# Kernel tuning notes

Measured on AMD Instinct MI355X. Metric: run time of the kernel, lower is better.

The kernel has to match this reference:

```python
import jax, jax.numpy as jnp
import numpy as np

N = 20000      # nodes
E = 320000     # edges (before self-loops)
IN = 128       # input_dim
HID = 64       # hidden_dim
HEADS = 4      # num_heads
SLOPE = 0.2    # PyG GATConv leaky_relu negative_slope


def setup_inputs() -> dict:
    key = jax.random.key(0)
    ks = jax.random.split(key, 20)
    g = lambda k, shape: jax.random.normal(k, shape, dtype=jnp.float32) * 0.1
    return {
        "x": jax.random.normal(ks[0], (N, IN), dtype=jnp.float32),
        "edge_index": jax.random.randint(ks[1], (2, E), 0, N),
        # layer 0: IN -> HID x HEADS, concat
        "lin0": g(ks[2], (IN, HEADS * HID)),
        "att_src0": g(ks[3], (HEADS, HID)),
        "att_dst0": g(ks[4], (HEADS, HID)),
        "bias0": g(ks[5], (HEADS * HID,)),
        # layer 1: HID*HEADS -> HID x HEADS, concat
        "lin1": g(ks[6], (HEADS * HID, HEADS * HID)),
        "att_src1": g(ks[7], (HEADS, HID)),
        "att_dst1": g(ks[8], (HEADS, HID)),
        "bias1": g(ks[9], (HEADS * HID,)),
        # layer 2: HID*HEADS -> HID, 1 head, mean (concat=False)
        "lin2": g(ks[10], (HEADS * HID, HID)),
        "att_src2": g(ks[11], (1, HID)),
        "att_dst2": g(ks[12], (1, HID)),
        "bias2": g(ks[13], (HID,)),
        # output MLP: HID -> HID//2 -> 1
        "w1": g(ks[14], (HID, HID // 2)),
        "b1": g(ks[15], (HID // 2,)),
        "w2": g(ks[16], (HID // 2, 1)),
        "b2": g(ks[17], (1,)),
    }


def _gat(x, src, dst, lin, att_src, att_dst, bias, heads, concat):
    n = x.shape[0]
    ch = att_src.shape[1]
    h = (x @ lin).reshape(n, heads, ch)                       # [N,H,C]
    a_s = jnp.sum(h * att_src, axis=-1)                       # [N,H]
    a_d = jnp.sum(h * att_dst, axis=-1)                       # [N,H]
    e = jax.nn.leaky_relu(a_s[src] + a_d[dst], negative_slope=SLOPE)  # [E,H]
    emax = jax.ops.segment_max(e, dst, num_segments=n)        # segment softmax over dst
    ee = jnp.exp(e - emax[dst])
    denom = jax.ops.segment_sum(ee, dst, num_segments=n)
    alpha = ee / denom[dst]                                   # [E,H]
    out = jax.ops.segment_sum(h[src] * alpha[:, :, None], dst, num_segments=n)  # [N,H,C]
    out = out.reshape(n, heads * ch) if concat else jnp.mean(out, axis=1)
    return out + bias


def reference(x, edge_index, lin0, att_src0, att_dst0, bias0,
              lin1, att_src1, att_dst1, bias1,
              lin2, att_src2, att_dst2, bias2,
              w1, b1, w2, b2):
    n = x.shape[0]
    loops = jnp.arange(n, dtype=edge_index.dtype)
    edge = jnp.concatenate([edge_index, jnp.stack([loops, loops])], axis=1)  # add self loops
    src, dst = edge[0], edge[1]
    h = jax.nn.elu(_gat(x, src, dst, lin0, att_src0, att_dst0, bias0, HEADS, True))
    h = jax.nn.elu(_gat(h, src, dst, lin1, att_src1, att_dst1, bias1, HEADS, True))
    h = jax.nn.elu(_gat(h, src, dst, lin2, att_src2, att_dst2, bias2, 1, False))
    h = jax.nn.relu(h @ w1 + b1)
    return h @ w2 + b2
```

## Files before the change

### kernel.cpp

```cpp
#include <hip/hip_runtime.h>

#define NNODES 20000
#define NEDGES 320000
#define SCAN_NB ((NNODES + 255) / 256)
#define DCAP 120

typedef __attribute__((ext_vector_type(8))) short bf16x8;
typedef __attribute__((ext_vector_type(4))) float f32x4;
typedef _Float16 f16x4 __attribute__((ext_vector_type(4)));
typedef _Float16 f16x8 __attribute__((ext_vector_type(8)));

__device__ __forceinline__ float leaky(float x) { return x > 0.f ? x : 0.2f * x; }
__device__ __forceinline__ float elu(float x) { return x > 0.f ? x : expm1f(x); }

__device__ __forceinline__ ushort f2bf(float f) {
  uint u = __float_as_uint(f);
  uint r = (u + 0x7fffu + ((u >> 16) & 1u)) >> 16;
  return (ushort)r;
}
__device__ __forceinline__ float bf2f(ushort h) {
  return __uint_as_float(((uint)h) << 16);
}

__device__ __forceinline__ void gll16(const ushort* g, ushort* l) {
  __builtin_amdgcn_global_load_lds((const __attribute__((address_space(1))) void*)g,
                                   (__attribute__((address_space(3))) void*)l, 16, 0, 0);
}

__global__ void k_hist(const int* __restrict__ dst, int* __restrict__ cnt, int e) {
  int i = blockIdx.x * blockDim.x + threadIdx.x;
  if (i < e) atomicAdd(&cnt[dst[i]], 1);
}

__global__ __launch_bounds__(256) void k_scan1(const int* __restrict__ cnt, int* __restrict__ row_start,
                                               int* __restrict__ blocksum, int n) {
  __shared__ int s[256];
  int t = threadIdx.x;
  int i = blockIdx.x * 256 + t;
  int v = (i < n) ? cnt[i] : 0;
  s[t] = v;
  __syncthreads();
  for (int off = 1; off < 256; off <<= 1) {
    int x = (t >= off) ? s[t - off] : 0;
    __syncthreads();
    s[t] += x;
    __syncthreads();
  }
  if (i < n) row_start[i] = s[t] - v;
  if (t == 255) blocksum[blockIdx.x] = s[255];
}

__global__ __launch_bounds__(128) void k_scan2(int* __restrict__ blocksum, int* __restrict__ blockoff,
                                               int* __restrict__ row_start, int nb, int n) {
  __shared__ int s[128];
  int t = threadIdx.x;
  int v = (t < nb) ? blocksum[t] : 0;
  s[t] = v;
  __syncthreads();
  for (int off = 1; off < 128; off <<= 1) {
    int x = (t >= off) ? s[t - off] : 0;
    __syncthreads();
    s[t] += x;
    __syncthreads();
  }
  if (t < nb) blockoff[t] = s[t] - v;
  if (t == nb - 1) row_start[n] = s[t];
}

__global__ __launch_bounds__(256) void k_scan3(int* __restrict__ row_start, const int* __restrict__ blockoff,
                                               int* __restrict__ fill, int n) {
  int i = blockIdx.x * 256 + threadIdx.x;
  if (i < n) {
    row_start[i] += blockoff[blockIdx.x];
    fill[i] = 0;
  }
}

__global__ void k_scatter(const int* __restrict__ src, const int* __restrict__ dst,
                          const int* __restrict__ row_start, int* __restrict__ fill,
                          int* __restrict__ csr, int e) {
  int i = blockIdx.x * blockDim.x + threadIdx.x;
  if (i < e) {
    int d = dst[i];
    int p = row_start[d] + atomicAdd(&fill[d], 1);
    csr[p] = src[i];
  }
}

__global__ void k_cvt_pack(const float* __restrict__ a, ushort* __restrict__ hi,
                           ushort* __restrict__ lo, int total, int* __restrict__ fill) {
  int i = blockIdx.x * blockDim.x + threadIdx.x;
  if (i < NNODES) fill[i] = 0;
  if (i >= total) return;
  const float* src = a + (size_t)i * 32;
  ushort h[32], lw[32];
#pragma unroll
  for (int r = 0; r < 32; r++) {
    int p = (r < 16) ? ((r >> 2) * 8 + (r & 3)) : (((r - 16) >> 2) * 8 + 4 + (r & 3));
    float v = src[r];
    ushort hh = f2bf(v);
    h[p] = hh;
    lw[p] = f2bf(v - bf2f(hh));
  }
  ushort* ho = hi + (size_t)i * 32;
  ushort* llo = lo + (size_t)i * 32;
#pragma unroll
  for (int q = 0; q < 4; q++) {
    *(bf16x8*)&ho[q * 8] = *(bf16x8*)&h[q * 8];
    *(bf16x8*)&llo[q * 8] = *(bf16x8*)&lw[q * 8];
  }
}

__device__ __forceinline__ void prep_w_one(const float* __restrict__ w, ushort* __restrict__ th,
                                           ushort* __restrict__ tl, int K, int OC, int idx) {
  int KC = K / 32;
  int oc = idx / KC, c = idx % KC;
  ushort h[32], lw[32];
#pragma unroll
  for (int r = 0; r < 32; r++) {
    int p = (r < 16) ? ((r >> 2) * 8 + (r & 3)) : (((r - 16) >> 2) * 8 + 4 + (r & 3));
    float v = w[(size_t)(c * 32 + r) * OC + oc];
    ushort hh = f2bf(v);
    h[p] = hh;
    lw[p] = f2bf(v - bf2f(hh));
  }
  ushort* ho = th + (size_t)oc * K + c * 32;
  ushort* llo = tl + (size_t)oc * K + c * 32;
#pragma unroll
  for (int q = 0; q < 4; q++) {
    *(bf16x8*)&ho[q * 8] = *(bf16x8*)&h[q * 8];
    *(bf16x8*)&llo[q * 8] = *(bf16x8*)&lw[q * 8];
  }
}

__global__ void k_prep_w3(const float* __restrict__ w0, const float* __restrict__ w1,
                          const float* __restrict__ w2,
                          ushort* __restrict__ th0, ushort* __restrict__ tl0,
                          ushort* __restrict__ th1, ushort* __restrict__ tl1,
                          ushort* __restrict__ th2, ushort* __restrict__ tl2) {
  int i = blockIdx.x * blockDim.x + threadIdx.x;
  if (i < 1024) prep_w_one(w0, th0, tl0, 128, 256, i);
  else if (i < 3072) prep_w_one(w1, th1, tl1, 256, 256, i - 1024);
  else if (i < 3584) prep_w_one(w2, th2, tl2, 256, 64, i - 3072);
}

template <int K, int NCT, int HEADS>
__global__ __launch_bounds__(256) void k_gemm_mfma(const ushort* __restrict__ Ah, const ushort* __restrict__ Al,
                                                   const ushort* __restrict__ Bh, const ushort* __restrict__ Bl,
                                                   const float* __restrict__ asrc, const float* __restrict__ adst,
                                                   _Float16* __restrict__ H, float* __restrict__ a_s,
                                                   float* __restrict__ a_d, int M, int OC) {
  constexpr int BM = 64, BN = NCT * 64, NC = K / 32;
  constexpr int ALO = 2048;
  constexpr int BOFF = 4096;
  constexpr int BLO = BOFF + BN * 32;
  constexpr int BUFE = BOFF + BN * 64;
  __shared__ ushort sb0[BUFE], sb1[BUFE];
  __shared__ float sh_s[4][64], sh_d[4][64];
  int w = threadIdx.x >> 6, l = threadIdx.x & 63;
  int n0 = blockIdx.x * BM;
  int cw = blockIdx.y * BN + w * (NCT * 16);
  int lr = l & 15;

  int q = l & 3;
  int srow = 16 * w + (l >> 2);
  int sgrow = min(n0 + srow, M - 1);
  int gA = q ^ ((srow >> 1) & 3);
  const ushort* aH = Ah + (size_t)sgrow * K + gA * 8;
  const ushort* aL = Al + (size_t)sgrow * K + gA * 8;
  const ushort* bH[NCT];
  const ushort* bL[NCT];
  int colb[NCT];
#pragma unroll
  for (int i = 0; i < NCT; i++) {
    colb[i] = 16 * NCT * w + 16 * i;
    int sc = colb[i] + (l >> 2);
    int gB = q ^ ((sc >> 1) & 3);
    bH[i] = Bh + (size_t)(blockIdx.y * BN + sc) * K + gB * 8;
    bL[i] = Bl + (size_t)(blockIdx.y * BN + sc) * K + gB * 8;
  }

#define STAGE(buf, c)                                              \
  {                                                                \
    gll16(aH + (c) * 32, &buf[0 + w * 512]);                       \
    gll16(aL + (c) * 32, &buf[ALO + w * 512]);                     \
    _Pragma("unroll") for (int i = 0; i < NCT; i++) {              \
      gll16(bH[i] + (c) * 32, &buf[BOFF + colb[i] * 32]);          \
      gll16(bL[i] + (c) * 32, &buf[BLO + colb[i] * 32]);           \
    }                                                              \
  }

  f32x4 acc[4][NCT];
#pragma unroll
  for (int r = 0; r < 4; r++)
#pragma unroll
    for (int t = 0; t < NCT; t++) acc[r][t] = (f32x4){0.f, 0.f, 0.f, 0.f};

#define COMP(buf)                                                                   \
  {                                                                                 \
    bf16x8 bhf[NCT], blf[NCT];                                                      \
    _Pragma("unroll") for (int t = 0; t < NCT; t++) {                               \
      int bcol = 16 * NCT * w + 16 * t + lr;                                        \
      int gb = (l >> 4) ^ ((bcol >> 1) & 3);                                        \
      bhf[t] = *(const bf16x8*)&buf[BOFF + bcol * 32 + gb * 8];                     \
      blf[t] = *(const bf16x8*)&buf[BLO + bcol * 32 + gb * 8];                      \
    }                                                                               \
    _Pragma("unroll") for (int r = 0; r < 4; r++) {                                 \
      int arow = 16 * r + lr;                                                       \
      int ga = (l >> 4) ^ ((arow >> 1) & 3);                                        \
      bf16x8 ahf = *(const bf16x8*)&buf[arow * 32 + ga * 8];                        \
      bf16x8 alf = *(const bf16x8*)&buf[ALO + arow * 32 + ga * 8];                  \
      _Pragma("unroll") for (int t = 0; t < NCT; t++) {                             \
        acc[r][t] = __builtin_amdgcn_mfma_f32_16x16x32_bf16(ahf, bhf[t], acc[r][t], 0, 0, 0); \
        acc[r][t] = __builtin_amdgcn_mfma_f32_16x16x32_bf16(alf, bhf[t], acc[r][t], 0, 0, 0); \
        acc[r][t] = __builtin_amdgcn_mfma_f32_16x16x32_bf16(ahf, blf[t], acc[r][t], 0, 0, 0); \
      }                                                                             \
    }                                                                               \
  }

  ushort* cur = sb0;
  ushort* nxt = sb1;
  STAGE(cur, 0);
  __syncthreads();
  for (int c = 0; c < NC; ++c) {
    if (c + 1 < NC) STAGE(nxt, c + 1);
    COMP(cur);
    __syncthreads();
    ushort* tmp = cur; cur = nxt; nxt = tmp;
  }
#undef STAGE
#undef COMP

#pragma unroll
  for (int r = 0; r < 4; r++)
#pragma unroll
    for (int t = 0; t < NCT; t++)
#pragma unroll
      for (int reg = 0; reg < 4; reg++) {
        int row = n0 + 16 * r + (l >> 4) * 4 + reg;
        if (row < M) H[(size_t)row * OC + cw + 16 * t + lr] = (_Float16)acc[r][t][reg];
      }

  float asv[NCT], adv[NCT];
#pragma unroll
  for (int t = 0; t < NCT; t++) {
    asv[t] = asrc[cw + 16 * t + lr];
    adv[t] = adst[cw + 16 * t + lr];
  }
#pragma unroll
  for (int r = 0; r < 4; r++) {
#pragma unroll
    for (int reg = 0; reg < 4; reg++) {
      float ps = 0.f, pd = 0.f;
#pragma unroll
      for (int t = 0; t < NCT; t++) {
        ps += acc[r][t][reg] * asv[t];
        pd += acc[r][t][reg] * adv[t];
      }
#pragma unroll
      for (int mask = 1; mask < 16; mask <<= 1) {
        ps += __shfl_xor(ps, mask, 64);
        pd += __shfl_xor(pd, mask, 64);
      }
      int rl = 16 * r + (l >> 4) * 4 + reg;
      if (lr == 0) { sh_s[w][rl] = ps; sh_d[w][rl] = pd; }
    }
  }
  __syncthreads();
  int tid = threadIdx.x;
  if (HEADS == 4) {
    if (tid < 128) {
      int rr = tid & 63, hl = tid >> 6;
      int row = n0 + rr;
      if (row < M) {
        int hidx = row * 4 + blockIdx.y * 2 + hl;
        a_s[hidx] = sh_s[2 * hl][rr] + sh_s[2 * hl + 1][rr];
        a_d[hidx] = sh_d[2 * hl][rr] + sh_d[2 * hl + 1][rr];
      }
    }
  } else {
    if (tid < 64) {
      int row = n0 + tid;
      if (row < M) {
        a_s[row] = sh_s[0][tid] + sh_s[1][tid] + sh_s[2][tid] + sh_s[3][tid];
        a_d[row] = sh_d[0][tid] + sh_d[1][tid] + sh_d[2][tid] + sh_d[3][tid];
      }
    }
  }
}

__global__ __launch_bounds__(256) void k_gat4(const _Float16* __restrict__ h, const float* __restrict__ a_s,
                                              const float* __restrict__ a_d, const int* __restrict__ row_start,
                                              const int* __restrict__ csr, const float* __restrict__ bias,
                                              ushort* __restrict__ Ah, ushort* __restrict__ Al) {
  __shared__ float elds[4][DCAP * 4];
  int wid = threadIdx.x >> 6, l = threadIdx.x & 63;
  int n = blockIdx.x * 4 + wid;
  if (n >= NNODES) return;
  int head = l >> 4, sub = l & 15;
  int half = l >> 5, sl = l & 31;
  int head2 = sl >> 3;
  int jb = row_start[n], je = row_start[n + 1];
  float ad = a_d[n * 4 + head];
  float es = leaky(a_s[n * 4 + head] + ad);
  float m = -1e30f, s = 0.f;
  if (sub == 0) { m = es; s = 1.f; }
  for (int j = jb + sub; j < je; j += 16) {
    float e = leaky(a_s[csr[j] * 4 + head] + ad);
    int o = j - jb;
    if (o < DCAP) elds[wid][o * 4 + head] = e;
    float nm = fmaxf(m, e);
    s = s * __expf(m - nm) + __expf(e - nm);
    m = nm;
  }
#pragma unroll
  for (int mask = 1; mask < 16; mask <<= 1) {
    float m2 = __shfl_xor(m, mask, 64);
    float s2 = __shfl_xor(s, mask, 64);
    float nm = fmaxf(m, m2);
    s = s * __expf(m - nm) + s2 * __expf(m2 - nm);
    m = nm;
  }
  __asm__ volatile("" ::: "memory");
  float inv = 1.f / s;
  float sa = __expf(es - m) * inv;
  int srcl = head2 << 4;
  float m2r = __shfl(m, srcl, 64);
  float inv2 = __shfl(inv, srcl, 64);
  float sa2 = __shfl(sa, srcl, 64);
  float ad2 = __shfl(ad, srcl, 64);

  float acc[8];
  f16x8 hv = *(const f16x8*)&h[(size_t)n * 256 + sl * 8];
#pragma unroll
  for (int i = 0; i < 8; i++) acc[i] = (half == 0) ? sa2 * (float)hv[i] : 0.f;

  int jcap = min(je, jb + DCAP);
  int j = jb;
  for (; j + 7 < jcap; j += 8) {
    int e0 = j + half, e1 = j + 2 + half, e2 = j + 4 + half, e3 = j + 6 + half;
    int s0 = csr[e0], s1 = csr[e1], s2 = csr[e2], s3 = csr[e3];
    float a0 = __expf(elds[wid][(e0 - jb) * 4 + head2] - m2r) * inv2;
    float a1 = __expf(elds[wid][(e1 - jb) * 4 + head2] - m2r) * inv2;
    float a2 = __expf(elds[wid][(e2 - jb) * 4 + head2] - m2r) * inv2;
    float a3 = __expf(elds[wid][(e3 - jb) * 4 + head2] - m2r) * inv2;
    f16x8 v0 = *(const f16x8*)&h[(size_t)s0 * 256 + sl * 8];
    f16x8 v1 = *(const f16x8*)&h[(size_t)s1 * 256 + sl * 8];
    f16x8 v2 = *(const f16x8*)&h[(size_t)s2 * 256 + sl * 8];
    f16x8 v3 = *(const f16x8*)&h[(size_t)s3 * 256 + sl * 8];
#pragma unroll
    for (int i = 0; i < 8; i++)
      acc[i] += a0 * (float)v0[i] + a1 * (float)v1[i] + a2 * (float)v2[i] + a3 * (float)v3[i];
  }
  for (; j + 1 < jcap; j += 2) {
    int e0 = j + half;
    int s0 = csr[e0];
    float a0 = __expf(elds[wid][(e0 - jb) * 4 + head2] - m2r) * inv2;
    f16x8 v0 = *(const f16x8*)&h[(size_t)s0 * 256 + sl * 8];
#pragma unroll
    for (int i = 0; i < 8; i++) acc[i] += a0 * (float)v0[i];
  }
  if (j < jcap) {
    int s0 = csr[j];
    float a0 = (half == 0) ? __expf(elds[wid][(j - jb) * 4 + head2] - m2r) * inv2 : 0.f;
    f16x8 v0 = *(const f16x8*)&h[(size_t)s0 * 256 + sl * 8];
#pragma unroll
    for (int i = 0; i < 8; i++) acc[i] += a0 * (float)v0[i];
    j++;
  }
  for (; j < je; j++) {
    int s0 = csr[j];
    float a0 = (half == 0) ? __expf(leaky(a_s[s0 * 4 + head2] + ad2) - m2r) * inv2 : 0.f;
    f16x8 v0 = *(const f16x8*)&h[(size_t)s0 * 256 + sl * 8];
#pragma unroll
    for (int i = 0; i < 8; i++) acc[i] += a0 * (float)v0[i];
  }
#pragma unroll
  for (int i = 0; i < 8; i++) acc[i] += __shfl_xor(acc[i], 32, 64);

  int c0 = sl * 8 + half * 4;
  int k = c0 & 31;
  size_t base = (size_t)n * 256 + (c0 >> 5) * 32 + ((k < 16) ? (k >> 2) * 8 : (((k - 16) >> 2) * 8 + 4));
  float4 b = *(const float4*)&bias[c0];
  int ai = half * 4;
  float o0 = elu(acc[ai + 0] + b.x);
  float o1 = elu(acc[ai + 1] + b.y);
  float o2 = elu(acc[ai + 2] + b.z);
  float o3 = elu(acc[ai + 3] + b.w);
  ushort4 hh, ll;
  hh.x = f2bf(o0); ll.x = f2bf(o0 - bf2f(hh.x));
  hh.y = f2bf(o1); ll.y = f2bf(o1 - bf2f(hh.y));
  hh.z = f2bf(o2); ll.z = f2bf(o2 - bf2f(hh.z));
  hh.w = f2bf(o3); ll.w = f2bf(o3 - bf2f(hh.w));
  *(ushort4*)&Ah[base] = hh;
  *(ushort4*)&Al[base] = ll;
}

__global__ __launch_bounds__(256) void k_gat1(const _Float16* __restrict__ h, const float* __restrict__ a_s,
                                              const float* __restrict__ a_d, const int* __restrict__ row_start,
                                              const int* __restrict__ csr, const float* __restrict__ bias,
                                              const float* __restrict__ w1, const float* __restrict__ b1,
                                              const float* __restrict__ w2, const float* __restrict__ b2,
                                              float* __restrict__ out) {
  __shared__ float elds[4][DCAP];
  __shared__ float sh[4][64];
  int wid = threadIdx.x >> 6, l = threadIdx.x & 63;
  int n = blockIdx.x * 4 + wid;
  int grp = l >> 4, cl = l & 15;
  float acc[4] = {0.f, 0.f, 0.f, 0.f};
  if (n < NNODES) {
    int jb = row_start[n], je = row_start[n + 1];
    float ad = a_d[n];
    float es = leaky(a_s[n] + ad);
    float m = -1e30f, s = 0.f;
    if (l == 0) { m = es; s = 1.f; }
    for (int j = jb + l; j < je; j += 64) {
      float e = leaky(a_s[csr[j]] + ad);
      int o = j - jb;
      if (o < DCAP) elds[wid][o] = e;
      float nm = fmaxf(m, e);
      s = s * __expf(m - nm) + __expf(e - nm);
      m = nm;
    }
#pragma unroll
    for (int mask = 1; mask < 64; mask <<= 1) {
      float m2 = __shfl_xor(m, mask, 64);
      float s2 = __shfl_xor(s, mask, 64);
      float nm = fmaxf(m, m2);
      s = s * __expf(m - nm) + s2 * __expf(m2 - nm);
      m = nm;
    }
    __asm__ volatile("" ::: "memory");
    float inv = 1.f / s;
    float sa = __expf(es - m) * inv;
    f16x4 hv = *(const f16x4*)&h[(size_t)n * 64 + cl * 4];
    if (grp == 0) {
#pragma unroll
      for (int i = 0; i < 4; i++) acc[i] = sa * (float)hv[i];
    }
    int jcap = min(je, jb + DCAP);
    int j = jb;
    for (; j + 7 < jcap; j += 8) {
      int e0 = j + grp, e1 = j + 4 + grp;
      int s0 = csr[e0], s1 = csr[e1];
      float a0 = __expf(elds[wid][e0 - jb] - m) * inv;
      float a1 = __expf(elds[wid][e1 - jb] - m) * inv;
      f16x4 v0 = *(const f16x4*)&h[(size_t)s0 * 64 + cl * 4];
      f16x4 v1 = *(const f16x4*)&h[(size_t)s1 * 64 + cl * 4];
#pragma unroll
      for (int i = 0; i < 4; i++) acc[i] += a0 * (float)v0[i] + a1 * (float)v1[i];
    }
    for (; j + 3 < jcap; j += 4) {
      int e0 = j + grp;
      int s0 = csr[e0];
      float a0 = __expf(elds[wid][e0 - jb] - m) * inv;
      f16x4 v0 = *(const f16x4*)&h[(size_t)s0 * 64 + cl * 4];
#pragma unroll
      for (int i = 0; i < 4; i++) acc[i] += a0 * (float)v0[i];
    }
    if (j + grp < jcap) {
      int e0 = j + grp;
      int s0 = csr[e0];
      float a0 = __expf(elds[wid][e0 - jb] - m) * inv;
      f16x4 v0 = *(const f16x4*)&h[(size_t)s0 * 64 + cl * 4];
#pragma unroll
      for (int i = 0; i < 4; i++) acc[i] += a0 * (float)v0[i];
    }
    for (int jj = jcap; jj < je; jj += 4) {
      int e0 = jj + grp;
      if (e0 < je) {
        int s0 = csr[e0];
        float a0 = __expf(leaky(a_s[s0] + ad) - m) * inv;
        f16x4 v0 = *(const f16x4*)&h[(size_t)s0 * 64 + cl * 4];
#pragma unroll
        for (int i = 0; i < 4; i++) acc[i] += a0 * (float)v0[i];
      }
    }
  }
#pragma unroll
  for (int i = 0; i < 4; i++) {
    acc[i] += __shfl_xor(acc[i], 16, 64);
    acc[i] += __shfl_xor(acc[i], 32, 64);
  }
  if (n < NNODES && l < 16) {
#pragma unroll
    for (int i = 0; i < 4; i++) sh[wid][cl * 4 + i] = elu(acc[i] + bias[cl * 4 + i]);
  }
  __syncthreads();
  float r = 0.f;
  if (l < 32 && n < NNODES) {
    r = b1[l];
#pragma unroll 8
    for (int k = 0; k < 64; k++) r += sh[wid][k] * w1[k * 32 + l];
    r = fmaxf(r, 0.f);
    r *= w2[l];
  }
  for (int mask = 16; mask >= 1; mask >>= 1) r += __shfl_xor(r, mask, 64);
  if (l == 0 && n < NNODES) out[n] = r + b2[0];
}

extern "C" void kernel_launch(void* const* d_in, const int* in_sizes, int n_in,
                              void* d_out, int out_size, void* d_ws, size_t ws_size,
                              hipStream_t stream) {
  const float* x    = (const float*)d_in[0];
  const int*   eidx = (const int*)d_in[1];
  const float* lin0 = (const float*)d_in[2];
  const float* as0  = (const float*)d_in[3];
  const float* ad0  = (const float*)d_in[4];
  const float* b0   = (const float*)d_in[5];
  const float* lin1 = (const float*)d_in[6];
  const float* as1  = (const float*)d_in[7];
  const float* ad1  = (const float*)d_in[8];
  const float* b1l  = (const float*)d_in[9];
  const float* lin2 = (const float*)d_in[10];
  const float* as2  = (const float*)d_in[11];
  const float* ad2  = (const float*)d_in[12];
  const float* b2l  = (const float*)d_in[13];
  const float* w1   = (const float*)d_in[14];
  const float* mb1  = (const float*)d_in[15];
  const float* w2   = (const float*)d_in[16];
  const float* mb2  = (const float*)d_in[17];
  float* outp = (float*)d_out;

  const int* srcA = eidx;
  const int* dstA = eidx + NEDGES;

  char* ws = (char*)d_ws;
  size_t o = 0;
  auto alloc = [&](size_t bytes) { size_t r = o; o += (bytes + 255) & ~255UL; return r; };
  _Float16* h16 = (_Float16*)(ws + alloc((size_t)NNODES * 256 * 2));
  ushort* Ahp = (ushort*)(ws + alloc((size_t)NNODES * 256 * 2));
  ushort* Alp = (ushort*)(ws + alloc((size_t)NNODES * 256 * 2));
  ushort* wh0 = (ushort*)(ws + alloc(128 * 256 * 2));
  ushort* wl0 = (ushort*)(ws + alloc(128 * 256 * 2));
  ushort* wh1 = (ushort*)(ws + alloc(256 * 256 * 2));
  ushort* wl1 = (ushort*)(ws + alloc(256 * 256 * 2));
  ushort* wh2 = (ushort*)(ws + alloc(256 * 64 * 2));
  ushort* wl2 = (ushort*)(ws + alloc(256 * 64 * 2));
  float*  vas = (float*)(ws + alloc((size_t)NNODES * 4 * 4));
  float*  vad = (float*)(ws + alloc((size_t)NNODES * 4 * 4));
  int* row_start = (int*)(ws + alloc((NNODES + 1) * 4));
  int* fill      = (int*)(ws + alloc(NNODES * 4));
  int* csr       = (int*)(ws + alloc(NEDGES * 4));
  int* blocksum  = (int*)(ws + alloc(SCAN_NB * 4));
  int* blockoff  = (int*)(ws + alloc(SCAN_NB * 4));

  k_cvt_pack<<<(NNODES * 4 + 255) / 256, 256, 0, stream>>>(x, Ahp, Alp, NNODES * 4, fill);
  k_prep_w3<<<(3584 + 255) / 256, 256, 0, stream>>>(lin0, lin1, lin2, wh0, wl0, wh1, wl1, wh2, wl2);

  k_hist<<<(NEDGES + 255) / 256, 256, 0, stream>>>(dstA, fill, NEDGES);
  k_scan1<<<SCAN_NB, 256, 0, stream>>>(fill, row_start, blocksum, NNODES);
  k_scan2<<<1, 128, 0, stream>>>(blocksum, blockoff, row_start, SCAN_NB, NNODES);
  k_scan3<<<SCAN_NB, 256, 0, stream>>>(row_start, blockoff, fill, NNODES);
  k_scatter<<<(NEDGES + 255) / 256, 256, 0, stream>>>(srcA, dstA, row_start, fill, csr, NEDGES);

  dim3 g44((NNODES + 63) / 64, 2);
  dim3 g21((NNODES + 63) / 64, 1);

  k_gemm_mfma<128, 2, 4><<<g44, 256, 0, stream>>>(Ahp, Alp, wh0, wl0, as0, ad0, h16, vas, vad, NNODES, 256);
  k_gat4<<<5000, 256, 0, stream>>>(h16, vas, vad, row_start, csr, b0, Ahp, Alp);

  k_gemm_mfma<256, 2, 4><<<g44, 256, 0, stream>>>(Ahp, Alp, wh1, wl1, as1, ad1, h16, vas, vad, NNODES, 256);
  k_gat4<<<5000, 256, 0, stream>>>(h16, vas, vad, row_start, csr, b1l, Ahp, Alp);

  k_gemm_mfma<256, 1, 1><<<g21, 256, 0, stream>>>(Ahp, Alp, wh2, wl2, as2, ad2, h16, vas, vad, NNODES, 64);
  k_gat1<<<5000, 256, 0, stream>>>(h16, vas, vad, row_start, csr, b2l, w1, mb1, w2, mb2, outp);
}
```

Before: 190.1 us.

## Replace split-bf16 three-pass GEMM with single fp16 MFMA and fuse prep kernels

Measured after the change: 182.0 us (median of 2 runs). 1.04x faster.

```diff
diff --git a/kernel.cpp b/kernel.cpp
--- a/kernel.cpp
+++ b/kernel.cpp
@@ -13,23 +13,9 @@
 __device__ __forceinline__ float leaky(float x) { return x > 0.f ? x : 0.2f * x; }
 __device__ __forceinline__ float elu(float x) { return x > 0.f ? x : expm1f(x); }
 
-__device__ __forceinline__ ushort f2bf(float f) {
-  uint u = __float_as_uint(f);
-  uint r = (u + 0x7fffu + ((u >> 16) & 1u)) >> 16;
-  return (ushort)r;
-}
-__device__ __forceinline__ float bf2f(ushort h) {
-  return __uint_as_float(((uint)h) << 16);
-}
-
 __device__ __forceinline__ void gll16(const ushort* g, ushort* l) {
   __builtin_amdgcn_global_load_lds((const __attribute__((address_space(1))) void*)g,
                                    (__attribute__((address_space(3))) void*)l, 16, 0, 0);
-}
-
-__global__ void k_hist(const int* __restrict__ dst, int* __restrict__ cnt, int e) {
-  int i = blockIdx.x * blockDim.x + threadIdx.x;
-  if (i < e) atomicAdd(&cnt[dst[i]], 1);
 }
 
 __global__ __launch_bounds__(256) void k_scan1(const int* __restrict__ cnt, int* __restrict__ row_start,
@@ -87,74 +73,57 @@
   }
 }
 
-__global__ void k_cvt_pack(const float* __restrict__ a, ushort* __restrict__ hi,
-                           ushort* __restrict__ lo, int total, int* __restrict__ fill) {
+__global__ void k_cvt_hist(const float* __restrict__ a, _Float16* __restrict__ Ap, int total,
+                           const int* __restrict__ dst, int* __restrict__ cnt, int e) {
+  int i = blockIdx.x * blockDim.x + threadIdx.x;
+  if (i < e) atomicAdd(&cnt[dst[i]], 1);
+  if (i >= total) return;
+  const float* src = a + (size_t)i * 32;
+  _Float16 h[32];
+#pragma unroll
+  for (int r = 0; r < 32; r++) {
+    int p = (r < 16) ? ((r >> 2) * 8 + (r & 3)) : (((r - 16) >> 2) * 8 + 4 + (r & 3));
+    h[p] = (_Float16)src[r];
+  }
+  _Float16* ho = Ap + (size_t)i * 32;
+#pragma unroll
+  for (int q = 0; q < 4; q++) *(f16x8*)&ho[q * 8] = *(f16x8*)&h[q * 8];
+}
+
+__device__ __forceinline__ void prep_w_one(const float* __restrict__ w, _Float16* __restrict__ th,
+                                           int K, int OC, int idx) {
+  int KC = K / 32;
+  int oc = idx / KC, c = idx % KC;
+  _Float16 h[32];
+#pragma unroll
+  for (int r = 0; r < 32; r++) {
+    int p = (r < 16) ? ((r >> 2) * 8 + (r & 3)) : (((r - 16) >> 2) * 8 + 4 + (r & 3));
+    h[p] = (_Float16)w[(size_t)(c * 32 + r) * OC + oc];
+  }
+  _Float16* ho = th + (size_t)oc * K + c * 32;
+#pragma unroll
+  for (int q = 0; q < 4; q++) *(f16x8*)&ho[q * 8] = *(f16x8*)&h[q * 8];
+}
+
+__global__ void k_prep_w3z(const float* __restrict__ w0, const float* __restrict__ w1,
+                           const float* __restrict__ w2,
+                           _Float16* __restrict__ th0, _Float16* __restrict__ th1,
+                           _Float16* __restrict__ th2, int* __restrict__ fill) {
   int i = blockIdx.x * blockDim.x + threadIdx.x;
   if (i < NNODES) fill[i] = 0;
-  if (i >= total) return;
-  const float* src = a + (size_t)i * 32;
-  ushort h[32], lw[32];
-#pragma unroll
-  for (int r = 0; r < 32; r++) {
-    int p = (r < 16) ? ((r >> 2) * 8 + (r & 3)) : (((r - 16) >> 2) * 8 + 4 + (r & 3));
-    float v = src[r];
-    ushort hh = f2bf(v);
-    h[p] = hh;
-    lw[p] = f2bf(v - bf2f(hh));
-  }
-  ushort* ho = hi + (size_t)i * 32;
-  ushort* llo = lo + (size_t)i * 32;
-#pragma unroll
-  for (int q = 0; q < 4; q++) {
-    *(bf16x8*)&ho[q * 8] = *(bf16x8*)&h[q * 8];
-    *(bf16x8*)&llo[q * 8] = *(bf16x8*)&lw[q * 8];
-  }
-}
-
-__device__ __forceinline__ void prep_w_one(const float* __restrict__ w, ushort* __restrict__ th,
-                                           ushort* __restrict__ tl, int K, int OC, int idx) {
-  int KC = K / 32;
-  int oc = idx / KC, c = idx % KC;
-  ushort h[32], lw[32];
-#pragma unroll
-  for (int r = 0; r < 32; r++) {
-    int p = (r < 16) ? ((r >> 2) * 8 + (r & 3)) : (((r - 16) >> 2) * 8 + 4 + (r & 3));
-    float v = w[(size_t)(c * 32 + r) * OC + oc];
-    ushort hh = f2bf(v);
-    h[p] = hh;
-    lw[p] = f2bf(v - bf2f(hh));
-  }
-  ushort* ho = th + (size_t)oc * K + c * 32;
-  ushort* llo = tl + (size_t)oc * K + c * 32;
-#pragma unroll
-  for (int q = 0; q < 4; q++) {
-    *(bf16x8*)&ho[q * 8] = *(bf16x8*)&h[q * 8];
-    *(bf16x8*)&llo[q * 8] = *(bf16x8*)&lw[q * 8];
-  }
-}
-
-__global__ void k_prep_w3(const float* __restrict__ w0, const float* __restrict__ w1,
-                          const float* __restrict__ w2,
-                          ushort* __restrict__ th0, ushort* __restrict__ tl0,
-                          ushort* __restrict__ th1, ushort* __restrict__ tl1,
-                          ushort* __restrict__ th2, ushort* __restrict__ tl2) {
-  int i = blockIdx.x * blockDim.x + threadIdx.x;
-  if (i < 1024) prep_w_one(w0, th0, tl0, 128, 256, i);
-  else if (i < 3072) prep_w_one(w1, th1, tl1, 256, 256, i - 1024);
-  else if (i < 3584) prep_w_one(w2, th2, tl2, 256, 64, i - 3072);
+  if (i < 1024) prep_w_one(w0, th0, 128, 256, i);
+  else if (i < 3072) prep_w_one(w1, th1, 256, 256, i - 1024);
+  else if (i < 3584) prep_w_one(w2, th2, 256, 64, i - 3072);
 }
 
 template <int K, int NCT, int HEADS>
-__global__ __launch_bounds__(256) void k_gemm_mfma(const ushort* __restrict__ Ah, const ushort* __restrict__ Al,
-                                                   const ushort* __restrict__ Bh, const ushort* __restrict__ Bl,
+__global__ __launch_bounds__(256) void k_gemm_mfma(const ushort* __restrict__ Ah, const ushort* __restrict__ Bh,
                                                    const float* __restrict__ asrc, const float* __restrict__ adst,
                                                    _Float16* __restrict__ H, float* __restrict__ a_s,
                                                    float* __restrict__ a_d, int M, int OC) {
   constexpr int BM = 64, BN = NCT * 64, NC = K / 32;
-  constexpr int ALO = 2048;
-  constexpr int BOFF = 4096;
-  constexpr int BLO = BOFF + BN * 32;
-  constexpr int BUFE = BOFF + BN * 64;
+  constexpr int BOFF = 2048;
+  constexpr int BUFE = BOFF + BN * 32;
   __shared__ ushort sb0[BUFE], sb1[BUFE];
   __shared__ float sh_s[4][64], sh_d[4][64];
   int w = threadIdx.x >> 6, l = threadIdx.x & 63;
@@ -167,9 +136,7 @@
   int sgrow = min(n0 + srow, M - 1);
   int gA = q ^ ((srow >> 1) & 3);
   const ushort* aH = Ah + (size_t)sgrow * K + gA * 8;
-  const ushort* aL = Al + (size_t)sgrow * K + gA * 8;
   const ushort* bH[NCT];
-  const ushort* bL[NCT];
   int colb[NCT];
 #pragma unroll
   for (int i = 0; i < NCT; i++) {
@@ -177,17 +144,13 @@
     int sc = colb[i] + (l >> 2);
     int gB = q ^ ((sc >> 1) & 3);
     bH[i] = Bh + (size_t)(blockIdx.y * BN + sc) * K + gB * 8;
-    bL[i] = Bl + (size_t)(blockIdx.y * BN + sc) * K + gB * 8;
   }
 
 #define STAGE(buf, c)                                              \
   {                                                                \
-    gll16(aH + (c) * 32, &buf[0 + w * 512]);                       \
-    gll16(aL + (c) * 32, &buf[ALO + w * 512]);                     \
-    _Pragma("unroll") for (int i = 0; i < NCT; i++) {              \
+    gll16(aH + (c) * 32, &buf[w * 512]);                           \
+    _Pragma("unroll") for (int i = 0; i < NCT; i++)                \
       gll16(bH[i] + (c) * 32, &buf[BOFF + colb[i] * 32]);          \
-      gll16(bL[i] + (c) * 32, &buf[BLO + colb[i] * 32]);           \
-    }                                                              \
   }
 
   f32x4 acc[4][NCT];
@@ -198,23 +161,18 @@
 
 #define COMP(buf)                                                                   \
   {                                                                                 \
-    bf16x8 bhf[NCT], blf[NCT];                                                      \
+    f16x8 bhf[NCT];                                                                 \
     _Pragma("unroll") for (int t = 0; t < NCT; t++) {                               \
       int bcol = 16 * NCT * w + 16 * t + lr;                                        \
       int gb = (l >> 4) ^ ((bcol >> 1) & 3);                                        \
-      bhf[t] = *(const bf16x8*)&buf[BOFF + bcol * 32 + gb * 8];                     \
-      blf[t] = *(const bf16x8*)&buf[BLO + bcol * 32 + gb * 8];                      \
+      bhf[t] = *(const f16x8*)&buf[BOFF + bcol * 32 + gb * 8];                      \
     }                                                                               \
     _Pragma("unroll") for (int r = 0; r < 4; r++) {                                 \
       int arow = 16 * r + lr;                                                       \
       int ga = (l >> 4) ^ ((arow >> 1) & 3);                                        \
-      bf16x8 ahf = *(const bf16x8*)&buf[arow * 32 + ga * 8];                        \
-      bf16x8 alf = *(const bf16x8*)&buf[ALO + arow * 32 + ga * 8];                  \
-      _Pragma("unroll") for (int t = 0; t < NCT; t++) {                             \
-        acc[r][t] = __builtin_amdgcn_mfma_f32_16x16x32_bf16(ahf, bhf[t], acc[r][t], 0, 0, 0); \
-        acc[r][t] = __builtin_amdgcn_mfma_f32_16x16x32_bf16(alf, bhf[t], acc[r][t], 0, 0, 0); \
-        acc[r][t] = __builtin_amdgcn_mfma_f32_16x16x32_bf16(ahf, blf[t], acc[r][t], 0, 0, 0); \
-      }                                                                             \
+      f16x8 ahf = *(const f16x8*)&buf[arow * 32 + ga * 8];                          \
+      _Pragma("unroll") for (int t = 0; t < NCT; t++)                               \
+        acc[r][t] = __builtin_amdgcn_mfma_f32_16x16x32_f16(ahf, bhf[t], acc[r][t], 0, 0, 0); \
     }                                                                               \
   }
 
@@ -292,7 +250,7 @@
 __global__ __launch_bounds__(256) void k_gat4(const _Float16* __restrict__ h, const float* __restrict__ a_s,
                                               const float* __restrict__ a_d, const int* __restrict__ row_start,
                                               const int* __restrict__ csr, const float* __restrict__ bias,
-                                              ushort* __restrict__ Ah, ushort* __restrict__ Al) {
+                                              _Float16* __restrict__ Ap) {
   __shared__ float elds[4][DCAP * 4];
   int wid = threadIdx.x >> 6, l = threadIdx.x & 63;
   int n = blockIdx.x * 4 + wid;
@@ -383,17 +341,12 @@
   size_t base = (size_t)n * 256 + (c0 >> 5) * 32 + ((k < 16) ? (k >> 2) * 8 : (((k - 16) >> 2) * 8 + 4));
   float4 b = *(const float4*)&bias[c0];
   int ai = half * 4;
-  float o0 = elu(acc[ai + 0] + b.x);
-  float o1 = elu(acc[ai + 1] + b.y);
-  float o2 = elu(acc[ai + 2] + b.z);
-  float o3 = elu(acc[ai + 3] + b.w);
-  ushort4 hh, ll;
-  hh.x = f2bf(o0); ll.x = f2bf(o0 - bf2f(hh.x));
-  hh.y = f2bf(o1); ll.y = f2bf(o1 - bf2f(hh.y));
-  hh.z = f2bf(o2); ll.z = f2bf(o2 - bf2f(hh.z));
-  hh.w = f2bf(o3); ll.w = f2bf(o3 - bf2f(hh.w));
-  *(ushort4*)&Ah[base] = hh;
-  *(ushort4*)&Al[base] = ll;
+  f16x4 pk;
+  pk[0] = (_Float16)elu(acc[ai + 0] + b.x);
+  pk[1] = (_Float16)elu(acc[ai + 1] + b.y);
+  pk[2] = (_Float16)elu(acc[ai + 2] + b.z);
+  pk[3] = (_Float16)elu(acc[ai + 3] + b.w);
+  *(f16x4*)&Ap[base] = pk;
 }
 
 __global__ __launch_bounds__(256) void k_gat1(const _Float16* __restrict__ h, const float* __restrict__ a_s,
@@ -529,14 +482,10 @@
   size_t o = 0;
   auto alloc = [&](size_t bytes) { size_t r = o; o += (bytes + 255) & ~255UL; return r; };
   _Float16* h16 = (_Float16*)(ws + alloc((size_t)NNODES * 256 * 2));
-  ushort* Ahp = (ushort*)(ws + alloc((size_t)NNODES * 256 * 2));
-  ushort* Alp = (ushort*)(ws + alloc((size_t)NNODES * 256 * 2));
-  ushort* wh0 = (ushort*)(ws + alloc(128 * 256 * 2));
-  ushort* wl0 = (ushort*)(ws + alloc(128 * 256 * 2));
-  ushort* wh1 = (ushort*)(ws + alloc(256 * 256 * 2));
-  ushort* wl1 = (ushort*)(ws + alloc(256 * 256 * 2));
-  ushort* wh2 = (ushort*)(ws + alloc(256 * 64 * 2));
-  ushort* wl2 = (ushort*)(ws + alloc(256 * 64 * 2));
+  _Float16* Ap  = (_Float16*)(ws + alloc((size_t)NNODES * 256 * 2));
+  _Float16* wh0 = (_Float16*)(ws + alloc(128 * 256 * 2));
+  _Float16* wh1 = (_Float16*)(ws + alloc(256 * 256 * 2));
+  _Float16* wh2 = (_Float16*)(ws + alloc(256 * 64 * 2));
   float*  vas = (float*)(ws + alloc((size_t)NNODES * 4 * 4));
   float*  vad = (float*)(ws + alloc((size_t)NNODES * 4 * 4));
   int* row_start = (int*)(ws + alloc((NNODES + 1) * 4));
@@ -545,10 +494,9 @@
   int* blocksum  = (int*)(ws + alloc(SCAN_NB * 4));
   int* blockoff  = (int*)(ws + alloc(SCAN_NB * 4));
 
-  k_cvt_pack<<<(NNODES * 4 + 255) / 256, 256, 0, stream>>>(x, Ahp, Alp, NNODES * 4, fill);
-  k_prep_w3<<<(3584 + 255) / 256, 256, 0, stream>>>(lin0, lin1, lin2, wh0, wl0, wh1, wl1, wh2, wl2);
-
-  k_hist<<<(NEDGES + 255) / 256, 256, 0, stream>>>(dstA, fill, NEDGES);
+  k_prep_w3z<<<(NNODES + 255) / 256, 256, 0, stream>>>(lin0, lin1, lin2, wh0, wh1, wh2, fill);
+  k_cvt_hist<<<(NEDGES + 255) / 256, 256, 0, stream>>>(x, Ap, NNODES * 4, dstA, fill, NEDGES);
+
   k_scan1<<<SCAN_NB, 256, 0, stream>>>(fill, row_start, blocksum, NNODES);
   k_scan2<<<1, 128, 0, stream>>>(blocksum, blockoff, row_start, SCAN_NB, NNODES);
   k_scan3<<<SCAN_NB, 256, 0, stream>>>(row_start, blockoff, fill, NNODES);
@@ -557,12 +505,12 @@
   dim3 g44((NNODES + 63) / 64, 2);
   dim3 g21((NNODES + 63) / 64, 1);
 
-  k_gemm_mfma<128, 2, 4><<<g44, 256, 0, stream>>>(Ahp, Alp, wh0, wl0, as0, ad0, h16, vas, vad, NNODES, 256);
-  k_gat4<<<5000, 256, 0, stream>>>(h16, vas, vad, row_start, csr, b0, Ahp, Alp);
-
-  k_gemm_mfma<256, 2, 4><<<g44, 256, 0, stream>>>(Ahp, Alp, wh1, wl1, as1, ad1, h16, vas, vad, NNODES, 256);
-  k_gat4<<<5000, 256, 0, stream>>>(h16, vas, vad, row_start, csr, b1l, Ahp, Alp);
-
-  k_gemm_mfma<256, 1, 1><<<g21, 256, 0, stream>>>(Ahp, Alp, wh2, wl2, as2, ad2, h16, vas, vad, NNODES, 64);
+  k_gemm_mfma<128, 2, 4><<<g44, 256, 0, stream>>>((const ushort*)Ap, (const ushort*)wh0, as0, ad0, h16, vas, vad, NNODES, 256);
+  k_gat4<<<5000, 256, 0, stream>>>(h16, vas, vad, row_start, csr, b0, Ap);
+
+  k_gemm_mfma<256, 2, 4><<<g44, 256, 0, stream>>>((const ushort*)Ap, (const ushort*)wh1, as1, ad1, h16, vas, vad, NNODES, 256);
+  k_gat4<<<5000, 256, 0, stream>>>(h16, vas, vad, row_start, csr, b1l, Ap);
+
+  k_gemm_mfma<256, 1, 1><<<g21, 256, 0, stream>>>((const ushort*)Ap, (const ushort*)wh2, as2, ad2, h16, vas, vad, NNODES, 64);
   k_gat1<<<5000, 256, 0, stream>>>(h16, vas, vad, row_start, csr, b2l, w1, mb1, w2, mb2, outp);
 }
```
